# Kernel tuning notes

Hardware: AMD Instinct MI355X
Metric: run time of the kernel (lower is better)

The kernel has to match this reference:

```python
import jax, jax.numpy as jnp
import numpy as np

T = 2048          # tokens
HIDDEN = 2048
FFN = 1024
E = 16            # routed experts
ZERO = 16         # zero experts
NTOT = E + ZERO   # router output dim
K = 4             # top-k
SCALE = 2.5       # routed_scaling_factor


def setup_inputs() -> dict:
    key = jax.random.key(0)
    k0, k1, k2, k3, k4 = jax.random.split(key, 5)
    return {
        "hidden_states": jax.random.normal(k0, (T, HIDDEN), jnp.float32),
        "router_w": jax.random.normal(k1, (NTOT, HIDDEN), jnp.float32) * 0.02,
        "e_score_correction_bias": jax.random.normal(k2, (NTOT,), jnp.float32) * 0.01,
        "w13": jax.random.normal(k3, (E, HIDDEN, 2 * FFN), jnp.float32) * 0.02,
        "w2": jax.random.normal(k4, (E, FFN, HIDDEN), jnp.float32) * 0.02,
    }


def reference(hidden_states, router_w, e_score_correction_bias, w13, w2):
    # ---- router: fp32 linear -> softmax -> bias-corrected top-k ----
    logits = hidden_states @ router_w.T                      # [T, NTOT]
    scores = jax.nn.softmax(logits, axis=-1)
    scores_for_choice = scores + e_score_correction_bias[None, :]
    topk_w, topk_ids = jax.lax.top_k(scores_for_choice, K)   # [T, K]
    topk_w = topk_w * SCALE

    # ---- zero-expert masking: ids >= E are identity experts ----
    zero_mask = topk_ids >= E
    zero_total = jnp.sum(jnp.where(zero_mask, topk_w, 0.0), axis=-1, keepdims=True)
    zero_expert_output = hidden_states * zero_total          # [T, HIDDEN]
    topk_ids = jnp.where(zero_mask, 0, topk_ids)
    topk_w = jnp.where(zero_mask, 0.0, topk_w)

    # ---- combine weights scattered to dense [T, E] (top-k ids unique per row;
    # masked duplicates at id 0 carry weight 0 so .add is exact) ----
    comb = jnp.zeros((hidden_states.shape[0], E), jnp.float32)
    comb = comb.at[jnp.arange(hidden_states.shape[0])[:, None], topk_ids].add(topk_w)

    # ---- grouped-GEMM experts expressed densely: gate_up -> swiglu -> down ----
    gate_up = jnp.einsum('th,ehf->tef', hidden_states, w13)  # [T, E, 2*FFN]
    gate, up = jnp.split(gate_up, 2, axis=-1)
    act = jax.nn.silu(gate) * up                             # npu_swiglu
    expert_out = jnp.einsum('tef,efh->teh', act, w2)         # [T, E, HIDDEN]

    routed = jnp.einsum('te,teh->th', comb, expert_out)
    return routed + zero_expert_output
```

## Files before the change

kernel.cpp:

```cpp
#include <hip/hip_runtime.h>
#include <hip/hip_bf16.h>
#include <math.h>

#define TOKENS 2048
#define HID 2048
#define FFN 1024
#define NEXP 16
#define NTOT 32
#define KSEL 4
#define RSCALE 2.5f

typedef __bf16 v8bf __attribute__((ext_vector_type(8)));
typedef float v4f __attribute__((ext_vector_type(4)));
typedef unsigned short u16x8v __attribute__((ext_vector_type(8)));

static __device__ __forceinline__ v8bf zero_v8bf() {
  u16x8v z = {0, 0, 0, 0, 0, 0, 0, 0};
  return __builtin_bit_cast(v8bf, z);
}

static __device__ __forceinline__ int swz(int row, int chunk) {
  return (row << 6) + ((((unsigned)(chunk ^ row)) & 7u) << 3);
}

__global__ __launch_bounds__(256) void router_kernel(
    const float* __restrict__ hidden, const float* __restrict__ rw,
    const float* __restrict__ bias, float* __restrict__ out,
    __bf16* __restrict__ hbf,
    int* __restrict__ counts, int* __restrict__ pair_token,
    float* __restrict__ pair_weight)
{
  const int t = blockIdx.x;
  const int tid = threadIdx.x;
  __shared__ float sh[HID];
  __shared__ float part[8][NTOT];
  __shared__ float s_zt;

  const float* hrow = hidden + (size_t)t * HID;
  for (int i = tid; i < HID / 4; i += 256)
    ((float4*)sh)[i] = ((const float4*)hrow)[i];
  __syncthreads();

  {
    const int base = tid * 8;
    v8bf v;
#pragma unroll
    for (int j = 0; j < 8; ++j) v[j] = (__bf16)sh[base + j];
    *(v8bf*)(hbf + (size_t)t * HID + base) = v;
  }

  {
    const int g = tid >> 5, e = tid & 31;
    const float* w = rw + (size_t)e * HID + g * 256;
    const float* hh = sh + g * 256;
    float acc = 0.f;
#pragma unroll 8
    for (int h = 0; h < 256; ++h) acc = fmaf(hh[h], w[h], acc);
    part[g][e] = acc;
  }
  __syncthreads();

  if (tid < 64) {
    const int lane = tid;
    float logit = -INFINITY;
    if (lane < NTOT) {
      float s = 0.f;
#pragma unroll
      for (int g = 0; g < 8; ++g) s += part[g][lane];
      logit = s;
    }
    float m = logit;
#pragma unroll
    for (int off = 32; off; off >>= 1) m = fmaxf(m, __shfl_xor(m, off));
    const float ex = (lane < NTOT) ? expf(logit - m) : 0.f;
    float sum = ex;
#pragma unroll
    for (int off = 32; off; off >>= 1) sum += __shfl_xor(sum, off);
    float sc = (lane < NTOT) ? (ex / sum + bias[lane]) : -INFINITY;

    float zt = 0.f;
#pragma unroll
    for (int it = 0; it < KSEL; ++it) {
      float v = sc; int vid = lane;
#pragma unroll
      for (int off = 32; off; off >>= 1) {
        const float ov = __shfl_xor(v, off);
        const int oid = __shfl_xor(vid, off);
        if (ov > v || (ov == v && oid < vid)) { v = ov; vid = oid; }
      }
      const float wv = v * RSCALE;
      if (vid >= NEXP) {
        zt += wv;
      } else if (lane == 0) {
        const int pos = atomicAdd(&counts[vid], 1);
        pair_token[vid * TOKENS + pos] = t;
        pair_weight[vid * TOKENS + pos] = wv;
      }
      if (lane == vid) sc = -INFINITY;
    }
    if (lane == 0) s_zt = zt;
  }
  __syncthreads();

  const float zt = s_zt;
  float* orow = out + (size_t)t * HID;
  for (int i = tid; i < HID / 4; i += 256) {
    float4 v = ((const float4*)sh)[i];
    v.x *= zt; v.y *= zt; v.z *= zt; v.w *= zt;
    ((float4*)orow)[i] = v;
  }
}

__global__ void scan_kernel(const int* __restrict__ counts,
                            int* __restrict__ offsets) {
  if (threadIdx.x == 0) {
    int acc = 0;
#pragma unroll
    for (int e = 0; e < NEXP; ++e) { offsets[e] = acc; acc += counts[e]; }
    offsets[NEXP] = acc;
  }
}

__global__ __launch_bounds__(256) void gemm1_kernel(
    const __bf16* __restrict__ hbf, const float* __restrict__ w13,
    const int* __restrict__ counts, const int* __restrict__ offsets,
    const int* __restrict__ pair_token, const float* __restrict__ pair_weight,
    __bf16* __restrict__ act)
{
  const int e = blockIdx.z, mt = blockIdx.y, nt = blockIdx.x;
  const int cnt = counts[e];
  const int m0 = mt * 128;
  if (m0 >= cnt) return;
  const int obase = offsets[e];

  __shared__ __bf16 sA[128 * 64];
  __shared__ __bf16 sBg[64 * 64];
  __shared__ __bf16 sBu[64 * 64];
  __shared__ int sTok[128];
  __shared__ float sW[128];

  const int tid = threadIdx.x;
  if (tid < 128) {
    const int m = m0 + tid;
    sTok[tid] = (m < cnt) ? pair_token[e * TOKENS + m] : -1;
    sW[tid] = (m < cnt) ? pair_weight[e * TOKENS + m] : 0.f;
  }
  __syncthreads();

  const float* w13e = w13 + (size_t)e * HID * (2 * FFN);
  const int fbase = nt * 64;

  const int wid = tid >> 6, lane = tid & 63;
  const int wr = wid >> 1, wf = wid & 1;
  const int lrow = lane & 15, lq = lane >> 4;

  const int ar = tid >> 1, ac4 = (tid & 1) * 4;
  const int a_tok = sTok[ar];
  const __bf16* a_src =
      (a_tok >= 0) ? (hbf + (size_t)a_tok * HID + ac4 * 8) : nullptr;

  v4f accg[4][2], accu[4][2];
#pragma unroll
  for (int mi = 0; mi < 4; ++mi)
#pragma unroll
    for (int fi = 0; fi < 2; ++fi) {
      v4f z = {0.f, 0.f, 0.f, 0.f};
      accg[mi][fi] = z; accu[mi][fi] = z;
    }

  for (int kt = 0; kt < HID; kt += 64) {
    if (a_tok >= 0) {
      const v8bf* s = (const v8bf*)(a_src + kt);
#pragma unroll
      for (int c = 0; c < 4; ++c)
        *(v8bf*)&sA[swz(ar, ac4 + c)] = s[c];
    } else {
#pragma unroll
      for (int c = 0; c < 4; ++c)
        *(v8bf*)&sA[swz(ar, ac4 + c)] = zero_v8bf();
    }
#pragma unroll
    for (int h = 0; h < 2; ++h) {
      __bf16* dst = h ? sBu : sBg;
#pragma unroll
      for (int ku = 0; ku < 2; ++ku) {
        const int kb = ku * 32 + wid * 8;
        const float* src =
            w13e + (size_t)(kt + kb) * (2 * FFN) + h * FFN + fbase + lane;
        v8bf v;
#pragma unroll
        for (int j = 0; j < 8; ++j) v[j] = (__bf16)src[(size_t)j * (2 * FFN)];
        *(v8bf*)&dst[swz(lane, ku * 4 + wid)] = v;
      }
    }
    __syncthreads();

#pragma unroll
    for (int ks = 0; ks < 2; ++ks) {
      v8bf a[4], bg[2], bu[2];
#pragma unroll
      for (int mi = 0; mi < 4; ++mi)
        a[mi] = *(const v8bf*)&sA[swz(wr * 64 + mi * 16 + lrow, ks * 4 + lq)];
#pragma unroll
      for (int fi = 0; fi < 2; ++fi) {
        bg[fi] = *(const v8bf*)&sBg[swz(wf * 32 + fi * 16 + lrow, ks * 4 + lq)];
        bu[fi] = *(const v8bf*)&sBu[swz(wf * 32 + fi * 16 + lrow, ks * 4 + lq)];
      }
#pragma unroll
      for (int mi = 0; mi < 4; ++mi)
#pragma unroll
        for (int fi = 0; fi < 2; ++fi) {
          accg[mi][fi] = __builtin_amdgcn_mfma_f32_16x16x32_bf16(
              a[mi], bg[fi], accg[mi][fi], 0, 0, 0);
          accu[mi][fi] = __builtin_amdgcn_mfma_f32_16x16x32_bf16(
              a[mi], bu[fi], accu[mi][fi], 0, 0, 0);
        }
    }
    __syncthreads();
  }

#pragma unroll
  for (int mi = 0; mi < 4; ++mi) {
#pragma unroll
    for (int fi = 0; fi < 2; ++fi) {
#pragma unroll
      for (int r = 0; r < 4; ++r) {
        const int lr = wr * 64 + mi * 16 + lq * 4 + r;
        const int m = m0 + lr;
        if (m < cnt) {
          const float g = accg[mi][fi][r];
          const float u = accu[mi][fi][r];
          const float sg = g / (1.f + __expf(-g));
          const float val = sg * u * sW[lr];
          const int f = fbase + wf * 32 + fi * 16 + lrow;
          act[(size_t)(obase + m) * FFN + f] = (__bf16)val;
        }
      }
    }
  }
}

__global__ __launch_bounds__(256) void gemm2_kernel(
    const __bf16* __restrict__ act, const float* __restrict__ w2,
    const int* __restrict__ counts, const int* __restrict__ offsets,
    const int* __restrict__ pair_token, float* __restrict__ out)
{
  const int e = blockIdx.z, mt = blockIdx.y, nt = blockIdx.x;
  const int cnt = counts[e];
  const int m0 = mt * 128;
  if (m0 >= cnt) return;
  const int obase = offsets[e];

  __shared__ __bf16 sA[128 * 64];
  __shared__ __bf16 sB[128 * 64];
  __shared__ int sTok[128];

  const int tid = threadIdx.x;
  if (tid < 128) {
    const int m = m0 + tid;
    sTok[tid] = (m < cnt) ? pair_token[e * TOKENS + m] : -1;
  }
  __syncthreads();

  const float* w2e = w2 + (size_t)e * FFN * HID;
  const int n0 = nt * 128;

  const int wid = tid >> 6, lane = tid & 63;
  const int wr = wid >> 1, wc = wid & 1;
  const int lrow = lane & 15, lq = lane >> 4;

  const int ar = tid >> 1, ac4 = (tid & 1) * 4;
  const bool avalid = (m0 + ar) < cnt;
  const __bf16* a_src = act + (size_t)(obase + m0 + ar) * FFN + ac4 * 8;

  v4f acc[4][4];
#pragma unroll
  for (int mi = 0; mi < 4; ++mi)
#pragma unroll
    for (int ni = 0; ni < 4; ++ni) {
      v4f z = {0.f, 0.f, 0.f, 0.f};
      acc[mi][ni] = z;
    }

  for (int kt = 0; kt < FFN; kt += 64) {
    if (avalid) {
      const v8bf* s = (const v8bf*)(a_src + kt);
#pragma unroll
      for (int c = 0; c < 4; ++c)
        *(v8bf*)&sA[swz(ar, ac4 + c)] = s[c];
    } else {
#pragma unroll
      for (int c = 0; c < 4; ++c)
        *(v8bf*)&sA[swz(ar, ac4 + c)] = zero_v8bf();
    }
#pragma unroll
    for (int nh = 0; nh < 2; ++nh) {
#pragma unroll
      for (int ku = 0; ku < 2; ++ku) {
        const int kb = ku * 32 + wid * 8;
        const float* src = w2e + (size_t)(kt + kb) * HID + n0 + nh * 64 + lane;
        v8bf v;
#pragma unroll
        for (int j = 0; j < 8; ++j) v[j] = (__bf16)src[(size_t)j * HID];
        *(v8bf*)&sB[swz(nh * 64 + lane, ku * 4 + wid)] = v;
      }
    }
    __syncthreads();

#pragma unroll
    for (int ks = 0; ks < 2; ++ks) {
      v8bf a[4], b[4];
#pragma unroll
      for (int mi = 0; mi < 4; ++mi)
        a[mi] = *(const v8bf*)&sA[swz(wr * 64 + mi * 16 + lrow, ks * 4 + lq)];
#pragma unroll
      for (int ni = 0; ni < 4; ++ni)
        b[ni] = *(const v8bf*)&sB[swz(wc * 64 + ni * 16 + lrow, ks * 4 + lq)];
#pragma unroll
      for (int mi = 0; mi < 4; ++mi)
#pragma unroll
        for (int ni = 0; ni < 4; ++ni)
          acc[mi][ni] = __builtin_amdgcn_mfma_f32_16x16x32_bf16(
              a[mi], b[ni], acc[mi][ni], 0, 0, 0);
    }
    __syncthreads();
  }

#pragma unroll
  for (int mi = 0; mi < 4; ++mi) {
#pragma unroll
    for (int ni = 0; ni < 4; ++ni) {
#pragma unroll
      for (int r = 0; r < 4; ++r) {
        const int lr = wr * 64 + mi * 16 + lq * 4 + r;
        const int m = m0 + lr;
        if (m < cnt) {
          const int t = sTok[lr];
          const int n = n0 + wc * 64 + ni * 16 + lrow;
          atomicAdd(&out[(size_t)t * HID + n], acc[mi][ni][r]);
        }
      }
    }
  }
}

extern "C" void kernel_launch(void* const* d_in, const int* in_sizes, int n_in,
                              void* d_out, int out_size, void* d_ws, size_t ws_size,
                              hipStream_t stream) {
  const float* hidden = (const float*)d_in[0];
  const float* rw     = (const float*)d_in[1];
  const float* bias   = (const float*)d_in[2];
  const float* w13    = (const float*)d_in[3];
  const float* w2     = (const float*)d_in[4];
  float* out = (float*)d_out;

  char* ws = (char*)d_ws;
  int* counts = (int*)ws;
  int* offsets = (int*)(ws + 64);
  int* pair_token = (int*)(ws + 256);
  float* pair_weight = (float*)(ws + 256 + (size_t)NEXP * TOKENS * 4);
  __bf16* hbf = (__bf16*)(ws + 256 + 2 * (size_t)NEXP * TOKENS * 4);
  __bf16* act = hbf + (size_t)TOKENS * HID;

  hipMemsetAsync(counts, 0, 16 * sizeof(int), stream);
  router_kernel<<<TOKENS, 256, 0, stream>>>(hidden, rw, bias, out, hbf,
                                            counts, pair_token, pair_weight);
  scan_kernel<<<1, 64, 0, stream>>>(counts, offsets);
  gemm1_kernel<<<dim3(FFN / 64, TOKENS / 128, NEXP), 256, 0, stream>>>(
      hbf, w13, counts, offsets, pair_token, pair_weight, act);
  gemm2_kernel<<<dim3(HID / 128, TOKENS / 128, NEXP), 256, 0, stream>>>(
      act, w2, counts, offsets, pair_token, out);
}
```

Measured before the change: 284.3 us.

## Double-buffer shared memory and prefetch next K-tile in both expert GEMMs

Both grouped GEMM kernels now use two LDS buffers and a register prefetch stage. Each iteration issues the global loads for the next K tile before running the MFMA work on the current tile, then writes the prefetched data into the other buffer, so only one barrier is needed per iteration. This aims to hide global memory latency, including the strided fp32 weight loads, behind the matrix math. In exchange it doubles LDS use, holds more prefetch registers, and adds a launch_bounds occupancy hint of 2 blocks, which could cause register spills.

```diff
diff --git a/kernel.cpp b/kernel.cpp
--- a/kernel.cpp
+++ b/kernel.cpp
@@ -121,7 +121,75 @@
   }
 }
 
-__global__ __launch_bounds__(256) void gemm1_kernel(
+
+static __device__ __forceinline__ void g1_load(
+    const __bf16* a_src, const float* b_base, int kt,
+    v8bf (&pa)[4], float (&pb)[2][2][8]) {
+  if (a_src) {
+    const v8bf* s = (const v8bf*)(a_src + kt);
+#pragma unroll
+    for (int c = 0; c < 4; ++c) pa[c] = s[c];
+  } else {
+#pragma unroll
+    for (int c = 0; c < 4; ++c) pa[c] = zero_v8bf();
+  }
+#pragma unroll
+  for (int h = 0; h < 2; ++h)
+#pragma unroll
+    for (int ku = 0; ku < 2; ++ku) {
+      const float* src = b_base + (size_t)(kt + ku * 32) * (2 * FFN) + h * FFN;
+#pragma unroll
+      for (int j = 0; j < 8; ++j) pb[h][ku][j] = src[(size_t)j * (2 * FFN)];
+    }
+}
+
+static __device__ __forceinline__ void g1_write(
+    __bf16* sA, __bf16* sBg, __bf16* sBu,
+    int ar, int ac4, int lane, int wid,
+    const v8bf (&pa)[4], const float (&pb)[2][2][8]) {
+#pragma unroll
+  for (int c = 0; c < 4; ++c) *(v8bf*)&sA[swz(ar, ac4 + c)] = pa[c];
+#pragma unroll
+  for (int h = 0; h < 2; ++h) {
+    __bf16* dst = h ? sBu : sBg;
+#pragma unroll
+    for (int ku = 0; ku < 2; ++ku) {
+      v8bf v;
+#pragma unroll
+      for (int j = 0; j < 8; ++j) v[j] = (__bf16)pb[h][ku][j];
+      *(v8bf*)&dst[swz(lane, ku * 4 + wid)] = v;
+    }
+  }
+}
+
+static __device__ __forceinline__ void g1_compute(
+    const __bf16* sA, const __bf16* sBg, const __bf16* sBu,
+    int wr, int wf, int lrow, int lq,
+    v4f (&accg)[4][2], v4f (&accu)[4][2]) {
+#pragma unroll
+  for (int ks = 0; ks < 2; ++ks) {
+    v8bf a[4], bg[2], bu[2];
+#pragma unroll
+    for (int mi = 0; mi < 4; ++mi)
+      a[mi] = *(const v8bf*)&sA[swz(wr * 64 + mi * 16 + lrow, ks * 4 + lq)];
+#pragma unroll
+    for (int fi = 0; fi < 2; ++fi) {
+      bg[fi] = *(const v8bf*)&sBg[swz(wf * 32 + fi * 16 + lrow, ks * 4 + lq)];
+      bu[fi] = *(const v8bf*)&sBu[swz(wf * 32 + fi * 16 + lrow, ks * 4 + lq)];
+    }
+#pragma unroll
+    for (int mi = 0; mi < 4; ++mi)
+#pragma unroll
+      for (int fi = 0; fi < 2; ++fi) {
+        accg[mi][fi] = __builtin_amdgcn_mfma_f32_16x16x32_bf16(
+            a[mi], bg[fi], accg[mi][fi], 0, 0, 0);
+        accu[mi][fi] = __builtin_amdgcn_mfma_f32_16x16x32_bf16(
+            a[mi], bu[fi], accu[mi][fi], 0, 0, 0);
+      }
+  }
+}
+
+__global__ __launch_bounds__(256, 2) void gemm1_kernel(
     const __bf16* __restrict__ hbf, const float* __restrict__ w13,
     const int* __restrict__ counts, const int* __restrict__ offsets,
     const int* __restrict__ pair_token, const float* __restrict__ pair_weight,
@@ -133,9 +201,9 @@
   if (m0 >= cnt) return;
   const int obase = offsets[e];
 
-  __shared__ __bf16 sA[128 * 64];
-  __shared__ __bf16 sBg[64 * 64];
-  __shared__ __bf16 sBu[64 * 64];
+  __shared__ __bf16 sA[2][128 * 64];
+  __shared__ __bf16 sBg[2][64 * 64];
+  __shared__ __bf16 sBu[2][64 * 64];
   __shared__ int sTok[128];
   __shared__ float sW[128];
 
@@ -158,6 +226,7 @@
   const int a_tok = sTok[ar];
   const __bf16* a_src =
       (a_tok >= 0) ? (hbf + (size_t)a_tok * HID + ac4 * 8) : nullptr;
+  const float* b_base = w13e + (size_t)(wid * 8) * (2 * FFN) + fbase + lane;
 
   v4f accg[4][2], accu[4][2];
 #pragma unroll
@@ -168,56 +237,23 @@
       accg[mi][fi] = z; accu[mi][fi] = z;
     }
 
-  for (int kt = 0; kt < HID; kt += 64) {
-    if (a_tok >= 0) {
-      const v8bf* s = (const v8bf*)(a_src + kt);
-#pragma unroll
-      for (int c = 0; c < 4; ++c)
-        *(v8bf*)&sA[swz(ar, ac4 + c)] = s[c];
-    } else {
-#pragma unroll
-      for (int c = 0; c < 4; ++c)
-        *(v8bf*)&sA[swz(ar, ac4 + c)] = zero_v8bf();
-    }
-#pragma unroll
-    for (int h = 0; h < 2; ++h) {
-      __bf16* dst = h ? sBu : sBg;
-#pragma unroll
-      for (int ku = 0; ku < 2; ++ku) {
-        const int kb = ku * 32 + wid * 8;
-        const float* src =
-            w13e + (size_t)(kt + kb) * (2 * FFN) + h * FFN + fbase + lane;
-        v8bf v;
-#pragma unroll
-        for (int j = 0; j < 8; ++j) v[j] = (__bf16)src[(size_t)j * (2 * FFN)];
-        *(v8bf*)&dst[swz(lane, ku * 4 + wid)] = v;
-      }
-    }
+  v8bf pa[4];
+  float pb[2][2][8];
+
+  g1_load(a_src, b_base, 0, pa, pb);
+  g1_write(sA[0], sBg[0], sBu[0], ar, ac4, lane, wid, pa, pb);
+  __syncthreads();
+
+  int cur = 0;
+  for (int kt = 64; kt < HID; kt += 64) {
+    g1_load(a_src, b_base, kt, pa, pb);
+    g1_compute(sA[cur], sBg[cur], sBu[cur], wr, wf, lrow, lq, accg, accu);
+    g1_write(sA[cur ^ 1], sBg[cur ^ 1], sBu[cur ^ 1],
+             ar, ac4, lane, wid, pa, pb);
     __syncthreads();
-
-#pragma unroll
-    for (int ks = 0; ks < 2; ++ks) {
-      v8bf a[4], bg[2], bu[2];
-#pragma unroll
-      for (int mi = 0; mi < 4; ++mi)
-        a[mi] = *(const v8bf*)&sA[swz(wr * 64 + mi * 16 + lrow, ks * 4 + lq)];
-#pragma unroll
-      for (int fi = 0; fi < 2; ++fi) {
-        bg[fi] = *(const v8bf*)&sBg[swz(wf * 32 + fi * 16 + lrow, ks * 4 + lq)];
-        bu[fi] = *(const v8bf*)&sBu[swz(wf * 32 + fi * 16 + lrow, ks * 4 + lq)];
-      }
-#pragma unroll
-      for (int mi = 0; mi < 4; ++mi)
-#pragma unroll
-        for (int fi = 0; fi < 2; ++fi) {
-          accg[mi][fi] = __builtin_amdgcn_mfma_f32_16x16x32_bf16(
-              a[mi], bg[fi], accg[mi][fi], 0, 0, 0);
-          accu[mi][fi] = __builtin_amdgcn_mfma_f32_16x16x32_bf16(
-              a[mi], bu[fi], accu[mi][fi], 0, 0, 0);
-        }
-    }
-    __syncthreads();
-  }
+    cur ^= 1;
+  }
+  g1_compute(sA[cur], sBg[cur], sBu[cur], wr, wf, lrow, lq, accg, accu);
 
 #pragma unroll
   for (int mi = 0; mi < 4; ++mi) {
@@ -240,7 +276,66 @@
   }
 }
 
-__global__ __launch_bounds__(256) void gemm2_kernel(
+
+static __device__ __forceinline__ void g2_load(
+    const __bf16* a_src, const float* b_base, int kt,
+    v8bf (&pa)[4], float (&pb)[2][2][8]) {
+  if (a_src) {
+    const v8bf* s = (const v8bf*)(a_src + kt);
+#pragma unroll
+    for (int c = 0; c < 4; ++c) pa[c] = s[c];
+  } else {
+#pragma unroll
+    for (int c = 0; c < 4; ++c) pa[c] = zero_v8bf();
+  }
+#pragma unroll
+  for (int nh = 0; nh < 2; ++nh)
+#pragma unroll
+    for (int ku = 0; ku < 2; ++ku) {
+      const float* src = b_base + (size_t)(kt + ku * 32) * HID + nh * 64;
+#pragma unroll
+      for (int j = 0; j < 8; ++j) pb[nh][ku][j] = src[(size_t)j * HID];
+    }
+}
+
+static __device__ __forceinline__ void g2_write(
+    __bf16* sA, __bf16* sB, int ar, int ac4, int lane, int wid,
+    const v8bf (&pa)[4], const float (&pb)[2][2][8]) {
+#pragma unroll
+  for (int c = 0; c < 4; ++c) *(v8bf*)&sA[swz(ar, ac4 + c)] = pa[c];
+#pragma unroll
+  for (int nh = 0; nh < 2; ++nh)
+#pragma unroll
+    for (int ku = 0; ku < 2; ++ku) {
+      v8bf v;
+#pragma unroll
+      for (int j = 0; j < 8; ++j) v[j] = (__bf16)pb[nh][ku][j];
+      *(v8bf*)&sB[swz(nh * 64 + lane, ku * 4 + wid)] = v;
+    }
+}
+
+static __device__ __forceinline__ void g2_compute(
+    const __bf16* sA, const __bf16* sB, int wr, int wc, int lrow, int lq,
+    v4f (&acc)[4][4]) {
+#pragma unroll
+  for (int ks = 0; ks < 2; ++ks) {
+    v8bf a[4], b[4];
+#pragma unroll
+    for (int mi = 0; mi < 4; ++mi)
+      a[mi] = *(const v8bf*)&sA[swz(wr * 64 + mi * 16 + lrow, ks * 4 + lq)];
+#pragma unroll
+    for (int ni = 0; ni < 4; ++ni)
+      b[ni] = *(const v8bf*)&sB[swz(wc * 64 + ni * 16 + lrow, ks * 4 + lq)];
+#pragma unroll
+    for (int mi = 0; mi < 4; ++mi)
+#pragma unroll
+      for (int ni = 0; ni < 4; ++ni)
+        acc[mi][ni] = __builtin_amdgcn_mfma_f32_16x16x32_bf16(
+            a[mi], b[ni], acc[mi][ni], 0, 0, 0);
+  }
+}
+
+__global__ __launch_bounds__(256, 2) void gemm2_kernel(
     const __bf16* __restrict__ act, const float* __restrict__ w2,
     const int* __restrict__ counts, const int* __restrict__ offsets,
     const int* __restrict__ pair_token, float* __restrict__ out)
@@ -251,8 +346,8 @@
   if (m0 >= cnt) return;
   const int obase = offsets[e];
 
-  __shared__ __bf16 sA[128 * 64];
-  __shared__ __bf16 sB[128 * 64];
+  __shared__ __bf16 sA[2][128 * 64];
+  __shared__ __bf16 sB[2][128 * 64];
   __shared__ int sTok[128];
 
   const int tid = threadIdx.x;
@@ -271,7 +366,9 @@
 
   const int ar = tid >> 1, ac4 = (tid & 1) * 4;
   const bool avalid = (m0 + ar) < cnt;
-  const __bf16* a_src = act + (size_t)(obase + m0 + ar) * FFN + ac4 * 8;
+  const __bf16* a_src =
+      avalid ? (act + (size_t)(obase + m0 + ar) * FFN + ac4 * 8) : nullptr;
+  const float* b_base = w2e + (size_t)(wid * 8) * HID + n0 + lane;
 
   v4f acc[4][4];
 #pragma unroll
@@ -282,49 +379,22 @@
       acc[mi][ni] = z;
     }
 
-  for (int kt = 0; kt < FFN; kt += 64) {
-    if (avalid) {
-      const v8bf* s = (const v8bf*)(a_src + kt);
-#pragma unroll
-      for (int c = 0; c < 4; ++c)
-        *(v8bf*)&sA[swz(ar, ac4 + c)] = s[c];
-    } else {
-#pragma unroll
-      for (int c = 0; c < 4; ++c)
-        *(v8bf*)&sA[swz(ar, ac4 + c)] = zero_v8bf();
-    }
-#pragma unroll
-    for (int nh = 0; nh < 2; ++nh) {
-#pragma unroll
-      for (int ku = 0; ku < 2; ++ku) {
-        const int kb = ku * 32 + wid * 8;
-        const float* src = w2e + (size_t)(kt + kb) * HID + n0 + nh * 64 + lane;
-        v8bf v;
-#pragma unroll
-        for (int j = 0; j < 8; ++j) v[j] = (__bf16)src[(size_t)j * HID];
-        *(v8bf*)&sB[swz(nh * 64 + lane, ku * 4 + wid)] = v;
-      }
-    }
+  v8bf pa[4];
+  float pb[2][2][8];
+
+  g2_load(a_src, b_base, 0, pa, pb);
+  g2_write(sA[0], sB[0], ar, ac4, lane, wid, pa, pb);
+  __syncthreads();
+
+  int cur = 0;
+  for (int kt = 64; kt < FFN; kt += 64) {
+    g2_load(a_src, b_base, kt, pa, pb);
+    g2_compute(sA[cur], sB[cur], wr, wc, lrow, lq, acc);
+    g2_write(sA[cur ^ 1], sB[cur ^ 1], ar, ac4, lane, wid, pa, pb);
     __syncthreads();
-
-#pragma unroll
-    for (int ks = 0; ks < 2; ++ks) {
-      v8bf a[4], b[4];
-#pragma unroll
-      for (int mi = 0; mi < 4; ++mi)
-        a[mi] = *(const v8bf*)&sA[swz(wr * 64 + mi * 16 + lrow, ks * 4 + lq)];
-#pragma unroll
-      for (int ni = 0; ni < 4; ++ni)
-        b[ni] = *(const v8bf*)&sB[swz(wc * 64 + ni * 16 + lrow, ks * 4 + lq)];
-#pragma unroll
-      for (int mi = 0; mi < 4; ++mi)
-#pragma unroll
-        for (int ni = 0; ni < 4; ++ni)
-          acc[mi][ni] = __builtin_amdgcn_mfma_f32_16x16x32_bf16(
-              a[mi], b[ni], acc[mi][ni], 0, 0, 0);
-    }
-    __syncthreads();
-  }
+    cur ^= 1;
+  }
+  g2_compute(sA[cur], sB[cur], wr, wc, lrow, lq, acc);
 
 #pragma unroll
   for (int mi = 0; mi < 4; ++mi) {
```

Result: slower. 299.7 us (+5.4%).

## Shrink GEMM N-tiles, reorder grid to M-fastest, and restructure B-tile loads

Applied to the files above, without the earlier changes.

Both expert GEMMs now use narrower N tiles: 32 FFN columns (gate+up) for gemm1 and 64 hidden columns for gemm2, with four-wave occupancy hints. The grid puts the M tile index in blockIdx.x, so consecutive blocks share the same weight columns and can reuse them in L2. Each thread now loads 16 fp32 weights from one column and converts them to two bf16 vectors. The goal is more blocks for better CU occupancy, given the uneven per-expert token counts, and better weight reuse. The cost is that each A tile is reloaded more often and the MFMA work per LDS load is lower.

```diff
diff --git a/kernel.cpp b/kernel.cpp
--- a/kernel.cpp
+++ b/kernel.cpp
@@ -121,21 +121,21 @@
   }
 }
 
-__global__ __launch_bounds__(256) void gemm1_kernel(
+__global__ __launch_bounds__(256, 4) void gemm1_kernel(
     const __bf16* __restrict__ hbf, const float* __restrict__ w13,
     const int* __restrict__ counts, const int* __restrict__ offsets,
     const int* __restrict__ pair_token, const float* __restrict__ pair_weight,
     __bf16* __restrict__ act)
 {
-  const int e = blockIdx.z, mt = blockIdx.y, nt = blockIdx.x;
+  const int e = blockIdx.z, mt = blockIdx.x, ft = blockIdx.y;
   const int cnt = counts[e];
   const int m0 = mt * 128;
   if (m0 >= cnt) return;
   const int obase = offsets[e];
+  const int fbase = ft * 32;
 
   __shared__ __bf16 sA[128 * 64];
-  __shared__ __bf16 sBg[64 * 64];
-  __shared__ __bf16 sBu[64 * 64];
+  __shared__ __bf16 sB[64 * 64];
   __shared__ int sTok[128];
   __shared__ float sW[128];
 
@@ -147,9 +147,6 @@
   }
   __syncthreads();
 
-  const float* w13e = w13 + (size_t)e * HID * (2 * FFN);
-  const int fbase = nt * 64;
-
   const int wid = tid >> 6, lane = tid & 63;
   const int wr = wid >> 1, wf = wid & 1;
   const int lrow = lane & 15, lq = lane >> 4;
@@ -159,100 +156,88 @@
   const __bf16* a_src =
       (a_tok >= 0) ? (hbf + (size_t)a_tok * HID + ac4 * 8) : nullptr;
 
-  v4f accg[4][2], accu[4][2];
-#pragma unroll
-  for (int mi = 0; mi < 4; ++mi)
-#pragma unroll
-    for (int fi = 0; fi < 2; ++fi) {
-      v4f z = {0.f, 0.f, 0.f, 0.f};
-      accg[mi][fi] = z; accu[mi][fi] = z;
-    }
+  const int f_off = lane & 31, h = lane >> 5;
+  const int brow = h * 32 + f_off;
+  const float* b_ptr = w13 + (size_t)e * HID * (2 * FFN)
+                     + (size_t)(wid * 16) * (2 * FFN) + h * FFN + fbase + f_off;
+
+  v4f accg[4], accu[4];
+#pragma unroll
+  for (int mi = 0; mi < 4; ++mi) {
+    v4f z = {0.f, 0.f, 0.f, 0.f};
+    accg[mi] = z; accu[mi] = z;
+  }
 
   for (int kt = 0; kt < HID; kt += 64) {
     if (a_tok >= 0) {
       const v8bf* s = (const v8bf*)(a_src + kt);
 #pragma unroll
-      for (int c = 0; c < 4; ++c)
-        *(v8bf*)&sA[swz(ar, ac4 + c)] = s[c];
+      for (int c = 0; c < 4; ++c) *(v8bf*)&sA[swz(ar, ac4 + c)] = s[c];
     } else {
 #pragma unroll
-      for (int c = 0; c < 4; ++c)
-        *(v8bf*)&sA[swz(ar, ac4 + c)] = zero_v8bf();
-    }
-#pragma unroll
-    for (int h = 0; h < 2; ++h) {
-      __bf16* dst = h ? sBu : sBg;
-#pragma unroll
-      for (int ku = 0; ku < 2; ++ku) {
-        const int kb = ku * 32 + wid * 8;
-        const float* src =
-            w13e + (size_t)(kt + kb) * (2 * FFN) + h * FFN + fbase + lane;
-        v8bf v;
-#pragma unroll
-        for (int j = 0; j < 8; ++j) v[j] = (__bf16)src[(size_t)j * (2 * FFN)];
-        *(v8bf*)&dst[swz(lane, ku * 4 + wid)] = v;
-      }
+      for (int c = 0; c < 4; ++c) *(v8bf*)&sA[swz(ar, ac4 + c)] = zero_v8bf();
+    }
+    {
+      const float* src = b_ptr + (size_t)kt * (2 * FFN);
+      float pb[16];
+#pragma unroll
+      for (int j = 0; j < 16; ++j) pb[j] = src[(size_t)j * (2 * FFN)];
+      v8bf v0, v1;
+#pragma unroll
+      for (int j = 0; j < 8; ++j) { v0[j] = (__bf16)pb[j]; v1[j] = (__bf16)pb[j + 8]; }
+      *(v8bf*)&sB[swz(brow, wid * 2)] = v0;
+      *(v8bf*)&sB[swz(brow, wid * 2 + 1)] = v1;
     }
     __syncthreads();
 
 #pragma unroll
     for (int ks = 0; ks < 2; ++ks) {
-      v8bf a[4], bg[2], bu[2];
+      v8bf a[4];
 #pragma unroll
       for (int mi = 0; mi < 4; ++mi)
         a[mi] = *(const v8bf*)&sA[swz(wr * 64 + mi * 16 + lrow, ks * 4 + lq)];
-#pragma unroll
-      for (int fi = 0; fi < 2; ++fi) {
-        bg[fi] = *(const v8bf*)&sBg[swz(wf * 32 + fi * 16 + lrow, ks * 4 + lq)];
-        bu[fi] = *(const v8bf*)&sBu[swz(wf * 32 + fi * 16 + lrow, ks * 4 + lq)];
-      }
-#pragma unroll
-      for (int mi = 0; mi < 4; ++mi)
-#pragma unroll
-        for (int fi = 0; fi < 2; ++fi) {
-          accg[mi][fi] = __builtin_amdgcn_mfma_f32_16x16x32_bf16(
-              a[mi], bg[fi], accg[mi][fi], 0, 0, 0);
-          accu[mi][fi] = __builtin_amdgcn_mfma_f32_16x16x32_bf16(
-              a[mi], bu[fi], accu[mi][fi], 0, 0, 0);
-        }
+      const v8bf bg = *(const v8bf*)&sB[swz(wf * 16 + lrow, ks * 4 + lq)];
+      const v8bf bu = *(const v8bf*)&sB[swz(32 + wf * 16 + lrow, ks * 4 + lq)];
+#pragma unroll
+      for (int mi = 0; mi < 4; ++mi) {
+        accg[mi] = __builtin_amdgcn_mfma_f32_16x16x32_bf16(a[mi], bg, accg[mi], 0, 0, 0);
+        accu[mi] = __builtin_amdgcn_mfma_f32_16x16x32_bf16(a[mi], bu, accu[mi], 0, 0, 0);
+      }
     }
     __syncthreads();
   }
 
+  const int f = fbase + wf * 16 + lrow;
 #pragma unroll
   for (int mi = 0; mi < 4; ++mi) {
 #pragma unroll
-    for (int fi = 0; fi < 2; ++fi) {
-#pragma unroll
-      for (int r = 0; r < 4; ++r) {
-        const int lr = wr * 64 + mi * 16 + lq * 4 + r;
-        const int m = m0 + lr;
-        if (m < cnt) {
-          const float g = accg[mi][fi][r];
-          const float u = accu[mi][fi][r];
-          const float sg = g / (1.f + __expf(-g));
-          const float val = sg * u * sW[lr];
-          const int f = fbase + wf * 32 + fi * 16 + lrow;
-          act[(size_t)(obase + m) * FFN + f] = (__bf16)val;
-        }
-      }
-    }
-  }
-}
-
-__global__ __launch_bounds__(256) void gemm2_kernel(
+    for (int r = 0; r < 4; ++r) {
+      const int lr = wr * 64 + mi * 16 + lq * 4 + r;
+      const int m = m0 + lr;
+      if (m < cnt) {
+        const float g = accg[mi][r];
+        const float u = accu[mi][r];
+        const float sg = g / (1.f + __expf(-g));
+        act[(size_t)(obase + m) * FFN + f] = (__bf16)(sg * u * sW[lr]);
+      }
+    }
+  }
+}
+
+__global__ __launch_bounds__(256, 4) void gemm2_kernel(
     const __bf16* __restrict__ act, const float* __restrict__ w2,
     const int* __restrict__ counts, const int* __restrict__ offsets,
     const int* __restrict__ pair_token, float* __restrict__ out)
 {
-  const int e = blockIdx.z, mt = blockIdx.y, nt = blockIdx.x;
+  const int e = blockIdx.z, mt = blockIdx.x, nt = blockIdx.y;
   const int cnt = counts[e];
   const int m0 = mt * 128;
   if (m0 >= cnt) return;
   const int obase = offsets[e];
+  const int n0 = nt * 64;
 
   __shared__ __bf16 sA[128 * 64];
-  __shared__ __bf16 sB[128 * 64];
+  __shared__ __bf16 sB[64 * 64];
   __shared__ int sTok[128];
 
   const int tid = threadIdx.x;
@@ -262,22 +247,23 @@
   }
   __syncthreads();
 
-  const float* w2e = w2 + (size_t)e * FFN * HID;
-  const int n0 = nt * 128;
-
   const int wid = tid >> 6, lane = tid & 63;
-  const int wr = wid >> 1, wc = wid & 1;
+  const int wr = wid >> 1, wf = wid & 1;
   const int lrow = lane & 15, lq = lane >> 4;
 
   const int ar = tid >> 1, ac4 = (tid & 1) * 4;
   const bool avalid = (m0 + ar) < cnt;
-  const __bf16* a_src = act + (size_t)(obase + m0 + ar) * FFN + ac4 * 8;
-
-  v4f acc[4][4];
+  const __bf16* a_src =
+      avalid ? (act + (size_t)(obase + m0 + ar) * FFN + ac4 * 8) : nullptr;
+
+  const float* b_ptr = w2 + (size_t)e * FFN * HID
+                     + (size_t)(wid * 16) * HID + n0 + lane;
+
+  v4f acc[4][2];
 #pragma unroll
   for (int mi = 0; mi < 4; ++mi)
 #pragma unroll
-    for (int ni = 0; ni < 4; ++ni) {
+    for (int ni = 0; ni < 2; ++ni) {
       v4f z = {0.f, 0.f, 0.f, 0.f};
       acc[mi][ni] = z;
     }
@@ -286,40 +272,37 @@
     if (avalid) {
       const v8bf* s = (const v8bf*)(a_src + kt);
 #pragma unroll
-      for (int c = 0; c < 4; ++c)
-        *(v8bf*)&sA[swz(ar, ac4 + c)] = s[c];
+      for (int c = 0; c < 4; ++c) *(v8bf*)&sA[swz(ar, ac4 + c)] = s[c];
     } else {
 #pragma unroll
-      for (int c = 0; c < 4; ++c)
-        *(v8bf*)&sA[swz(ar, ac4 + c)] = zero_v8bf();
-    }
-#pragma unroll
-    for (int nh = 0; nh < 2; ++nh) {
-#pragma unroll
-      for (int ku = 0; ku < 2; ++ku) {
-        const int kb = ku * 32 + wid * 8;
-        const float* src = w2e + (size_t)(kt + kb) * HID + n0 + nh * 64 + lane;
-        v8bf v;
-#pragma unroll
-        for (int j = 0; j < 8; ++j) v[j] = (__bf16)src[(size_t)j * HID];
-        *(v8bf*)&sB[swz(nh * 64 + lane, ku * 4 + wid)] = v;
-      }
+      for (int c = 0; c < 4; ++c) *(v8bf*)&sA[swz(ar, ac4 + c)] = zero_v8bf();
+    }
+    {
+      const float* src = b_ptr + (size_t)kt * HID;
+      float pb[16];
+#pragma unroll
+      for (int j = 0; j < 16; ++j) pb[j] = src[(size_t)j * HID];
+      v8bf v0, v1;
+#pragma unroll
+      for (int j = 0; j < 8; ++j) { v0[j] = (__bf16)pb[j]; v1[j] = (__bf16)pb[j + 8]; }
+      *(v8bf*)&sB[swz(lane, wid * 2)] = v0;
+      *(v8bf*)&sB[swz(lane, wid * 2 + 1)] = v1;
     }
     __syncthreads();
 
 #pragma unroll
     for (int ks = 0; ks < 2; ++ks) {
-      v8bf a[4], b[4];
+      v8bf a[4], b[2];
 #pragma unroll
       for (int mi = 0; mi < 4; ++mi)
         a[mi] = *(const v8bf*)&sA[swz(wr * 64 + mi * 16 + lrow, ks * 4 + lq)];
 #pragma unroll
-      for (int ni = 0; ni < 4; ++ni)
-        b[ni] = *(const v8bf*)&sB[swz(wc * 64 + ni * 16 + lrow, ks * 4 + lq)];
+      for (int ni = 0; ni < 2; ++ni)
+        b[ni] = *(const v8bf*)&sB[swz(wf * 32 + ni * 16 + lrow, ks * 4 + lq)];
 #pragma unroll
       for (int mi = 0; mi < 4; ++mi)
 #pragma unroll
-        for (int ni = 0; ni < 4; ++ni)
+        for (int ni = 0; ni < 2; ++ni)
           acc[mi][ni] = __builtin_amdgcn_mfma_f32_16x16x32_bf16(
               a[mi], b[ni], acc[mi][ni], 0, 0, 0);
     }
@@ -329,14 +312,14 @@
 #pragma unroll
   for (int mi = 0; mi < 4; ++mi) {
 #pragma unroll
-    for (int ni = 0; ni < 4; ++ni) {
+    for (int ni = 0; ni < 2; ++ni) {
 #pragma unroll
       for (int r = 0; r < 4; ++r) {
         const int lr = wr * 64 + mi * 16 + lq * 4 + r;
         const int m = m0 + lr;
         if (m < cnt) {
           const int t = sTok[lr];
-          const int n = n0 + wc * 64 + ni * 16 + lrow;
+          const int n = n0 + wf * 32 + ni * 16 + lrow;
           atomicAdd(&out[(size_t)t * HID + n], acc[mi][ni][r]);
         }
       }
@@ -366,8 +349,8 @@
   router_kernel<<<TOKENS, 256, 0, stream>>>(hidden, rw, bias, out, hbf,
                                             counts, pair_token, pair_weight);
   scan_kernel<<<1, 64, 0, stream>>>(counts, offsets);
-  gemm1_kernel<<<dim3(FFN / 64, TOKENS / 128, NEXP), 256, 0, stream>>>(
+  gemm1_kernel<<<dim3(16, FFN / 32, NEXP), 256, 0, stream>>>(
       hbf, w13, counts, offsets, pair_token, pair_weight, act);
-  gemm2_kernel<<<dim3(HID / 128, TOKENS / 128, NEXP), 256, 0, stream>>>(
+  gemm2_kernel<<<dim3(16, HID / 64, NEXP), 256, 0, stream>>>(
       act, w2, counts, offsets, pair_token, out);
 }
```

After: 913.6 us. 221% more time.
